# Optimization experiments

Hardware: AMD Instinct MI355X
Metric: run time of the kernel (lower is better)

Reference implementation:

```python
import jax, jax.numpy as jnp
import numpy as np

N_NODES = 40000


def gcn_conv(x, edge_index, W, b, num_nodes):
    """PyG GCNConv: add self-loops, sym-normalize, x @ W.T then scatter-add, + bias."""
    src = edge_index[0]
    dst = edge_index[1]
    loop = jnp.arange(num_nodes, dtype=src.dtype)
    src = jnp.concatenate([src, loop])
    dst = jnp.concatenate([dst, loop])
    # linear transform first (PyG applies lin before propagate)
    h = x @ W.T  # [N, out]
    # symmetric normalization: deg over destination (with self-loops)
    deg = jax.ops.segment_sum(jnp.ones_like(dst, dtype=h.dtype), dst, num_segments=num_nodes)
    dinv = jnp.where(deg > 0, jax.lax.rsqrt(deg), 0.0)
    norm = dinv[src] * dinv[dst]  # [E+N]
    msg = h[src] * norm[:, None]  # gather + scale
    out = jax.ops.segment_sum(msg, dst, num_segments=num_nodes)  # scatter-add
    return out + b


def setup_inputs() -> dict:
    key = jax.random.key(0)
    k1, k2, k3, k4, k5, k6, k7 = jax.random.split(key, 7)
    C, H, F_out = 128, 128, 1
    E = 640000
    x = jax.random.normal(k1, (N_NODES, C), dtype=jnp.float32)
    edge_index = jax.random.randint(k2, (2, E), 0, N_NODES, dtype=jnp.int64)
    # Glorot-ish init for conv weights (PyG lin.weight shape [out, in]), zero bias
    W1 = jax.random.normal(k3, (H, C), dtype=jnp.float32) / np.sqrt(C)
    b1 = jnp.zeros((H,), dtype=jnp.float32)
    W2 = jax.random.normal(k4, (F_out, H), dtype=jnp.float32) / np.sqrt(H)
    b2 = jnp.zeros((F_out,), dtype=jnp.float32)
    return {"x": x, "edge_index": edge_index, "W1": W1, "b1": b1, "W2": W2, "b2": b2}


def reference(x, edge_index, W1, b1, W2, b2):
    h = gcn_conv(x, edge_index, W1, b1, N_NODES)
    h = jax.nn.relu(h)
    out = gcn_conv(h, edge_index, W2, b2, N_NODES)
    return jax.nn.sigmoid(out)
```

## Files before the change

### kernel.cpp

```cpp
#include <hip/hip_runtime.h>
#include <math.h>
#include <stdint.h>

#define FDIM 128
#define CAP 64

typedef __bf16 bf16x8 __attribute__((ext_vector_type(8)));
typedef float f32x4 __attribute__((ext_vector_type(4)));

__device__ __forceinline__ ushort f2bf(float f) {
    uint32_t u = __float_as_uint(f);
    uint32_t r = (u >> 16) & 1;
    return (ushort)((u + 0x7fffu + r) >> 16);
}


__global__ __launch_bounds__(256) void k_zero4(int4* __restrict__ p, int n4) {
    int i = blockIdx.x * blockDim.x + threadIdx.x;
    int stride = gridDim.x * blockDim.x;
    for (; i < n4; i += stride) p[i] = make_int4(0, 0, 0, 0);
}

__global__ __launch_bounds__(256) void k_scatter_ell(const int* __restrict__ src,
                                                     const int* __restrict__ dst,
                                                     int* __restrict__ cnt,
                                                     ushort* __restrict__ ell, int E) {
    int e = blockIdx.x * blockDim.x + threadIdx.x;
    if (e < E) {
        int d = dst[e];
        int p = atomicAdd(&cnt[d], 1);
        if (p < CAP) ell[(size_t)d * CAP + p] = (ushort)src[e];
    }
}


#define XS 136

__global__ __launch_bounds__(256) void k_linear1_mfma(const float* __restrict__ x,
                                                      const float* __restrict__ W,
                                                      const int* __restrict__ cnt,
                                                      ushort* __restrict__ h, int n) {
    __shared__ __align__(16) ushort Wl[128 * XS];
    __shared__ __align__(16) ushort Xl[64 * XS];

    int tid = threadIdx.x;
    int node0 = blockIdx.x * 64;

#pragma unroll
    for (int i = 0; i < 16; ++i) {
        int q = tid + i * 256;
        int j = q >> 5;
        int c0 = (q & 31) * 4;
        float4 v = *(const float4*)(W + (size_t)q * 4);
        uint2 p;
        p.x = (uint32_t)f2bf(v.x) | ((uint32_t)f2bf(v.y) << 16);
        p.y = (uint32_t)f2bf(v.z) | ((uint32_t)f2bf(v.w) << 16);
        *(uint2*)&Wl[j * XS + c0] = p;
    }
#pragma unroll
    for (int i = 0; i < 8; ++i) {
        int q = tid + i * 256;
        int r = q >> 5;
        int c0 = (q & 31) * 4;
        int gr = node0 + r;
        float4 v = make_float4(0.f, 0.f, 0.f, 0.f);
        float s = 0.f;
        if (gr < n) {
            v = *(const float4*)(x + (size_t)gr * FDIM + c0);
            s = rsqrtf((float)cnt[gr] + 1.0f);
        }
        uint2 p;
        p.x = (uint32_t)f2bf(v.x * s) | ((uint32_t)f2bf(v.y * s) << 16);
        p.y = (uint32_t)f2bf(v.z * s) | ((uint32_t)f2bf(v.w * s) << 16);
        *(uint2*)&Xl[r * XS + c0] = p;
    }
    __syncthreads();

    int lane = tid & 63, wid = tid >> 6;
    int m0 = (wid >> 1) * 32;
    int j0 = (wid & 1) * 64;
    int lrow = lane & 15, kg = lane >> 4;

    bf16x8 af[2][4];
#pragma unroll
    for (int mt = 0; mt < 2; ++mt)
#pragma unroll
        for (int ks = 0; ks < 4; ++ks)
            af[mt][ks] = *(const bf16x8*)&Xl[(m0 + mt * 16 + lrow) * XS + ks * 32 + kg * 8];

    f32x4 acc[2][4] = {};
#pragma unroll
    for (int jt = 0; jt < 4; ++jt) {
        bf16x8 bfr[4];
#pragma unroll
        for (int ks = 0; ks < 4; ++ks)
            bfr[ks] = *(const bf16x8*)&Wl[(j0 + jt * 16 + lrow) * XS + ks * 32 + kg * 8];
#pragma unroll
        for (int mt = 0; mt < 2; ++mt)
#pragma unroll
            for (int ks = 0; ks < 4; ++ks)
                acc[mt][jt] = __builtin_amdgcn_mfma_f32_16x16x32_bf16(
                    af[mt][ks], bfr[ks], acc[mt][jt], 0, 0, 0);
    }

#pragma unroll
    for (int mt = 0; mt < 2; ++mt)
#pragma unroll
        for (int jt = 0; jt < 4; ++jt)
#pragma unroll
            for (int r = 0; r < 4; ++r) {
                int gi = node0 + m0 + mt * 16 + kg * 4 + r;
                int gj = j0 + jt * 16 + lrow;
                if (gi < n) h[(size_t)gi * FDIM + gj] = f2bf(acc[mt][jt][r]);
            }
}


__device__ __forceinline__ float bf_lo(uint32_t u) { return __uint_as_float(u << 16); }
__device__ __forceinline__ float bf_hi(uint32_t u) { return __uint_as_float(u & 0xFFFF0000u); }

__global__ __launch_bounds__(256) void k_agg1_h2(const uint32_t* __restrict__ h,
                                                 const ushort* __restrict__ ell,
                                                 const int* __restrict__ cnt,
                                                 const float* __restrict__ b1,
                                                 const float* __restrict__ W2,
                                                 float* __restrict__ h2s, int n) {
    int gtid = blockIdx.x * blockDim.x + threadIdx.x;
    int d = gtid >> 6;
    int lane = threadIdx.x & 63;
    if (d >= n) return;

    int degt = cnt[d];
    int deg = min(degt, CAP);
    int myidx = (lane < deg) ? (int)ell[(size_t)d * CAP + lane] : 0;

    uint32_t u = h[(size_t)d * 64 + lane];
    float ax[8], ay[8];
    ax[0] = bf_lo(u); ay[0] = bf_hi(u);
#pragma unroll
    for (int r = 1; r < 8; ++r) { ax[r] = 0.f; ay[r] = 0.f; }

    int k = 0;
    for (; k + 7 < deg; k += 8) {
        int s[8];
        uint32_t uu[8];
#pragma unroll
        for (int r = 0; r < 8; ++r) s[r] = __shfl(myidx, k + r);
#pragma unroll
        for (int r = 0; r < 8; ++r) uu[r] = h[(size_t)s[r] * 64 + lane];
#pragma unroll
        for (int r = 0; r < 8; ++r) { ax[r] += bf_lo(uu[r]); ay[r] += bf_hi(uu[r]); }
    }
    for (; k + 3 < deg; k += 4) {
        int s[4];
        uint32_t uu[4];
#pragma unroll
        for (int r = 0; r < 4; ++r) s[r] = __shfl(myidx, k + r);
#pragma unroll
        for (int r = 0; r < 4; ++r) uu[r] = h[(size_t)s[r] * 64 + lane];
#pragma unroll
        for (int r = 0; r < 4; ++r) { ax[r] += bf_lo(uu[r]); ay[r] += bf_hi(uu[r]); }
    }
    for (; k < deg; ++k) {
        int s0 = __shfl(myidx, k);
        uint32_t u0 = h[(size_t)s0 * 64 + lane];
        ax[0] += bf_lo(u0); ay[0] += bf_hi(u0);
    }

    float sx = ((ax[0] + ax[1]) + (ax[2] + ax[3])) + ((ax[4] + ax[5]) + (ax[6] + ax[7]));
    float sy = ((ay[0] + ay[1]) + (ay[2] + ay[3])) + ((ay[4] + ay[5]) + (ay[6] + ay[7]));

    float dd = rsqrtf((float)degt + 1.0f);
    float ox = sx * dd;
    float oy = sy * dd;

    float2 bb = *(const float2*)(b1 + lane * 2);
    float2 ww = *(const float2*)(W2 + lane * 2);
    float s = fmaxf(ox + bb.x, 0.f) * ww.x + fmaxf(oy + bb.y, 0.f) * ww.y;
#pragma unroll
    for (int o = 32; o; o >>= 1) s += __shfl_down(s, o);
    if (lane == 0) h2s[d] = s * dd;
}


__global__ __launch_bounds__(256) void k_agg2(const float* __restrict__ h2s,
                                              const ushort* __restrict__ ell,
                                              const int* __restrict__ cnt,
                                              const float* __restrict__ b2,
                                              float* __restrict__ out, int n) {
    int gtid = blockIdx.x * blockDim.x + threadIdx.x;
    int i = gtid >> 6;
    int lane = threadIdx.x & 63;
    if (i >= n) return;

    int degt = cnt[i];
    int deg = min(degt, CAP);
    float v = 0.f;
    if (lane < deg) {
        int s = ell[(size_t)i * CAP + lane];
        v = h2s[s];
    }
#pragma unroll
    for (int o = 32; o; o >>= 1) v += __shfl_down(v, o);
    if (lane == 0) {
        float dd = rsqrtf((float)degt + 1.0f);
        float r = (h2s[i] + v) * dd + b2[0];
        out[i] = 1.f / (1.f + expf(-r));
    }
}


extern "C" void kernel_launch(void* const* d_in, const int* in_sizes, int n_in,
                              void* d_out, int out_size, void* d_ws, size_t ws_size,
                              hipStream_t stream) {
    const float* x  = (const float*)d_in[0];
    const int*   ei = (const int*)d_in[1];
    const float* W1 = (const float*)d_in[2];
    const float* b1 = (const float*)d_in[3];
    const float* W2 = (const float*)d_in[4];
    const float* b2 = (const float*)d_in[5];

    int n = out_size;
    int E = in_sizes[1] / 2;
    const int* src = ei;
    const int* dst = ei + E;

    char* w = (char*)d_ws;
    int*    cnt = (int*)w;     w += (size_t)((n + 3) & ~3) * 4;
    ushort* ell = (ushort*)w;  w += (size_t)n * CAP * 2;
    ushort* h1s = (ushort*)w;  w += (size_t)n * FDIM * 2;
    float*  h2s = (float*)w;   w += (size_t)n * 4;

    int n4 = ((n + 3) & ~3) / 4;

    k_zero4<<<40, 256, 0, stream>>>((int4*)cnt, n4);
    k_scatter_ell<<<(E + 255) / 256, 256, 0, stream>>>(src, dst, cnt, ell, E);
    k_linear1_mfma<<<(n + 63) / 64, 256, 0, stream>>>(x, W1, cnt, h1s, n);
    k_agg1_h2<<<(n * 64 + 255) / 256, 256, 0, stream>>>((const uint32_t*)h1s, ell, cnt, b1, W2, h2s, n);
    k_agg2<<<(n * 64 + 255) / 256, 256, 0, stream>>>(h2s, ell, cnt, b2, (float*)d_out, n);
}
```

Measured before the change: 85.38 us.

## Fold count zeroing into linear kernel, move source normalization into aggregation

Zeroing the degree counters now happens inside the linear kernel, which also drops its dependence on counts and runs before the edge scatter. The per-source degree scaling moves from the linear stage into the first aggregation kernel, where each lane gathers its neighbour's count and shares it by shuffle. The linear kernel now handles two 64-node tiles per block so each staged W tile is reused. The scatter kernel reads four edges per thread with vector loads. The aim is to remove one launch and break the count dependency; the cost is an extra per-edge count gather and multiply in aggregation.

```diff
diff --git a/kernel.cpp b/kernel.cpp
--- a/kernel.cpp
+++ b/kernel.cpp
@@ -15,36 +15,21 @@
 }
 
 
-__global__ __launch_bounds__(256) void k_zero4(int4* __restrict__ p, int n4) {
-    int i = blockIdx.x * blockDim.x + threadIdx.x;
-    int stride = gridDim.x * blockDim.x;
-    for (; i < n4; i += stride) p[i] = make_int4(0, 0, 0, 0);
-}
-
-__global__ __launch_bounds__(256) void k_scatter_ell(const int* __restrict__ src,
-                                                     const int* __restrict__ dst,
-                                                     int* __restrict__ cnt,
-                                                     ushort* __restrict__ ell, int E) {
-    int e = blockIdx.x * blockDim.x + threadIdx.x;
-    if (e < E) {
-        int d = dst[e];
-        int p = atomicAdd(&cnt[d], 1);
-        if (p < CAP) ell[(size_t)d * CAP + p] = (ushort)src[e];
-    }
-}
-
-
 #define XS 136
 
 __global__ __launch_bounds__(256) void k_linear1_mfma(const float* __restrict__ x,
                                                       const float* __restrict__ W,
-                                                      const int* __restrict__ cnt,
+                                                      int* __restrict__ cnt,
                                                       ushort* __restrict__ h, int n) {
     __shared__ __align__(16) ushort Wl[128 * XS];
     __shared__ __align__(16) ushort Xl[64 * XS];
 
     int tid = threadIdx.x;
-    int node0 = blockIdx.x * 64;
+
+    if (tid < 128) {
+        int g = blockIdx.x * 128 + tid;
+        if (g < n) cnt[g] = 0;
+    }
 
 #pragma unroll
     for (int i = 0; i < 16; ++i) {
@@ -57,62 +42,89 @@
         p.y = (uint32_t)f2bf(v.z) | ((uint32_t)f2bf(v.w) << 16);
         *(uint2*)&Wl[j * XS + c0] = p;
     }
-#pragma unroll
-    for (int i = 0; i < 8; ++i) {
-        int q = tid + i * 256;
-        int r = q >> 5;
-        int c0 = (q & 31) * 4;
-        int gr = node0 + r;
-        float4 v = make_float4(0.f, 0.f, 0.f, 0.f);
-        float s = 0.f;
-        if (gr < n) {
-            v = *(const float4*)(x + (size_t)gr * FDIM + c0);
-            s = rsqrtf((float)cnt[gr] + 1.0f);
-        }
-        uint2 p;
-        p.x = (uint32_t)f2bf(v.x * s) | ((uint32_t)f2bf(v.y * s) << 16);
-        p.y = (uint32_t)f2bf(v.z * s) | ((uint32_t)f2bf(v.w * s) << 16);
-        *(uint2*)&Xl[r * XS + c0] = p;
-    }
-    __syncthreads();
 
     int lane = tid & 63, wid = tid >> 6;
     int m0 = (wid >> 1) * 32;
     int j0 = (wid & 1) * 64;
     int lrow = lane & 15, kg = lane >> 4;
 
-    bf16x8 af[2][4];
-#pragma unroll
-    for (int mt = 0; mt < 2; ++mt)
-#pragma unroll
-        for (int ks = 0; ks < 4; ++ks)
-            af[mt][ks] = *(const bf16x8*)&Xl[(m0 + mt * 16 + lrow) * XS + ks * 32 + kg * 8];
-
-    f32x4 acc[2][4] = {};
-#pragma unroll
-    for (int jt = 0; jt < 4; ++jt) {
-        bf16x8 bfr[4];
-#pragma unroll
-        for (int ks = 0; ks < 4; ++ks)
-            bfr[ks] = *(const bf16x8*)&Wl[(j0 + jt * 16 + lrow) * XS + ks * 32 + kg * 8];
+    for (int t = 0; t < 2; ++t) {
+        int node0 = blockIdx.x * 128 + t * 64;
+        if (node0 >= n) break;
+
+        __syncthreads();
+#pragma unroll
+        for (int i = 0; i < 8; ++i) {
+            int q = tid + i * 256;
+            int r = q >> 5;
+            int c0 = (q & 31) * 4;
+            int gr = node0 + r;
+            float4 v = make_float4(0.f, 0.f, 0.f, 0.f);
+            if (gr < n) v = *(const float4*)(x + (size_t)gr * FDIM + c0);
+            uint2 p;
+            p.x = (uint32_t)f2bf(v.x) | ((uint32_t)f2bf(v.y) << 16);
+            p.y = (uint32_t)f2bf(v.z) | ((uint32_t)f2bf(v.w) << 16);
+            *(uint2*)&Xl[r * XS + c0] = p;
+        }
+        __syncthreads();
+
+        bf16x8 af[2][4];
 #pragma unroll
         for (int mt = 0; mt < 2; ++mt)
 #pragma unroll
             for (int ks = 0; ks < 4; ++ks)
-                acc[mt][jt] = __builtin_amdgcn_mfma_f32_16x16x32_bf16(
-                    af[mt][ks], bfr[ks], acc[mt][jt], 0, 0, 0);
-    }
-
-#pragma unroll
-    for (int mt = 0; mt < 2; ++mt)
-#pragma unroll
-        for (int jt = 0; jt < 4; ++jt)
-#pragma unroll
-            for (int r = 0; r < 4; ++r) {
-                int gi = node0 + m0 + mt * 16 + kg * 4 + r;
-                int gj = j0 + jt * 16 + lrow;
-                if (gi < n) h[(size_t)gi * FDIM + gj] = f2bf(acc[mt][jt][r]);
-            }
+                af[mt][ks] = *(const bf16x8*)&Xl[(m0 + mt * 16 + lrow) * XS + ks * 32 + kg * 8];
+
+        f32x4 acc[2][4] = {};
+#pragma unroll
+        for (int jt = 0; jt < 4; ++jt) {
+            bf16x8 bfr[4];
+#pragma unroll
+            for (int ks = 0; ks < 4; ++ks)
+                bfr[ks] = *(const bf16x8*)&Wl[(j0 + jt * 16 + lrow) * XS + ks * 32 + kg * 8];
+#pragma unroll
+            for (int mt = 0; mt < 2; ++mt)
+#pragma unroll
+                for (int ks = 0; ks < 4; ++ks)
+                    acc[mt][jt] = __builtin_amdgcn_mfma_f32_16x16x32_bf16(
+                        af[mt][ks], bfr[ks], acc[mt][jt], 0, 0, 0);
+        }
+
+#pragma unroll
+        for (int mt = 0; mt < 2; ++mt)
+#pragma unroll
+            for (int jt = 0; jt < 4; ++jt)
+#pragma unroll
+                for (int r = 0; r < 4; ++r) {
+                    int gi = node0 + m0 + mt * 16 + kg * 4 + r;
+                    int gj = j0 + jt * 16 + lrow;
+                    if (gi < n) h[(size_t)gi * FDIM + gj] = f2bf(acc[mt][jt][r]);
+                }
+    }
+}
+
+
+__global__ __launch_bounds__(256) void k_scatter_ell(const int* __restrict__ src,
+                                                     const int* __restrict__ dst,
+                                                     int* __restrict__ cnt,
+                                                     ushort* __restrict__ ell, int E) {
+    int i = blockIdx.x * blockDim.x + threadIdx.x;
+    int base = i * 4;
+    if (base + 3 < E) {
+        int4 s4 = *(const int4*)(src + base);
+        int4 d4 = *(const int4*)(dst + base);
+        int p;
+        p = atomicAdd(&cnt[d4.x], 1); if (p < CAP) ell[(size_t)d4.x * CAP + p] = (ushort)s4.x;
+        p = atomicAdd(&cnt[d4.y], 1); if (p < CAP) ell[(size_t)d4.y * CAP + p] = (ushort)s4.y;
+        p = atomicAdd(&cnt[d4.z], 1); if (p < CAP) ell[(size_t)d4.z * CAP + p] = (ushort)s4.z;
+        p = atomicAdd(&cnt[d4.w], 1); if (p < CAP) ell[(size_t)d4.w * CAP + p] = (ushort)s4.w;
+    } else {
+        for (int e = base; e < E; ++e) {
+            int d = dst[e];
+            int p = atomicAdd(&cnt[d], 1);
+            if (p < CAP) ell[(size_t)d * CAP + p] = (ushort)src[e];
+        }
+    }
 }
 
 
@@ -132,45 +144,49 @@
 
     int degt = cnt[d];
     int deg = min(degt, CAP);
-    int myidx = (lane < deg) ? (int)ell[(size_t)d * CAP + lane] : 0;
-
+    int myidx = 0;
+    float mydv = 0.f;
+    if (lane < deg) {
+        myidx = (int)ell[(size_t)d * CAP + lane];
+        mydv = rsqrtf((float)cnt[myidx] + 1.0f);
+    }
+
+    float dd = rsqrtf((float)degt + 1.0f);
     uint32_t u = h[(size_t)d * 64 + lane];
     float ax[8], ay[8];
-    ax[0] = bf_lo(u); ay[0] = bf_hi(u);
+    ax[0] = bf_lo(u) * dd; ay[0] = bf_hi(u) * dd;
 #pragma unroll
     for (int r = 1; r < 8; ++r) { ax[r] = 0.f; ay[r] = 0.f; }
 
     int k = 0;
     for (; k + 7 < deg; k += 8) {
-        int s[8];
-        uint32_t uu[8];
-#pragma unroll
-        for (int r = 0; r < 8; ++r) s[r] = __shfl(myidx, k + r);
+        int s[8]; float dv[8]; uint32_t uu[8];
+#pragma unroll
+        for (int r = 0; r < 8; ++r) { s[r] = __shfl(myidx, k + r); dv[r] = __shfl(mydv, k + r); }
 #pragma unroll
         for (int r = 0; r < 8; ++r) uu[r] = h[(size_t)s[r] * 64 + lane];
 #pragma unroll
-        for (int r = 0; r < 8; ++r) { ax[r] += bf_lo(uu[r]); ay[r] += bf_hi(uu[r]); }
+        for (int r = 0; r < 8; ++r) { ax[r] += bf_lo(uu[r]) * dv[r]; ay[r] += bf_hi(uu[r]) * dv[r]; }
     }
     for (; k + 3 < deg; k += 4) {
-        int s[4];
-        uint32_t uu[4];
-#pragma unroll
-        for (int r = 0; r < 4; ++r) s[r] = __shfl(myidx, k + r);
+        int s[4]; float dv[4]; uint32_t uu[4];
+#pragma unroll
+        for (int r = 0; r < 4; ++r) { s[r] = __shfl(myidx, k + r); dv[r] = __shfl(mydv, k + r); }
 #pragma unroll
         for (int r = 0; r < 4; ++r) uu[r] = h[(size_t)s[r] * 64 + lane];
 #pragma unroll
-        for (int r = 0; r < 4; ++r) { ax[r] += bf_lo(uu[r]); ay[r] += bf_hi(uu[r]); }
+        for (int r = 0; r < 4; ++r) { ax[r] += bf_lo(uu[r]) * dv[r]; ay[r] += bf_hi(uu[r]) * dv[r]; }
     }
     for (; k < deg; ++k) {
         int s0 = __shfl(myidx, k);
+        float dv0 = __shfl(mydv, k);
         uint32_t u0 = h[(size_t)s0 * 64 + lane];
-        ax[0] += bf_lo(u0); ay[0] += bf_hi(u0);
+        ax[0] += bf_lo(u0) * dv0; ay[0] += bf_hi(u0) * dv0;
     }
 
     float sx = ((ax[0] + ax[1]) + (ax[2] + ax[3])) + ((ax[4] + ax[5]) + (ax[6] + ax[7]));
     float sy = ((ay[0] + ay[1]) + (ay[2] + ay[3])) + ((ay[4] + ay[5]) + (ay[6] + ay[7]));
 
-    float dd = rsqrtf((float)degt + 1.0f);
     float ox = sx * dd;
     float oy = sy * dd;
 
@@ -231,11 +247,11 @@
     ushort* h1s = (ushort*)w;  w += (size_t)n * FDIM * 2;
     float*  h2s = (float*)w;   w += (size_t)n * 4;
 
-    int n4 = ((n + 3) & ~3) / 4;
-
-    k_zero4<<<40, 256, 0, stream>>>((int4*)cnt, n4);
-    k_scatter_ell<<<(E + 255) / 256, 256, 0, stream>>>(src, dst, cnt, ell, E);
-    k_linear1_mfma<<<(n + 63) / 64, 256, 0, stream>>>(x, W1, cnt, h1s, n);
+    int nblk_lin = (n + 127) / 128;
+    int nblk_sc  = (E / 4 + 255) / 256;
+
+    k_linear1_mfma<<<nblk_lin, 256, 0, stream>>>(x, W1, cnt, h1s, n);
+    k_scatter_ell<<<nblk_sc, 256, 0, stream>>>(src, dst, cnt, ell, E);
     k_agg1_h2<<<(n * 64 + 255) / 256, 256, 0, stream>>>((const uint32_t*)h1s, ell, cnt, b1, W2, h2s, n);
     k_agg2<<<(n * 64 + 255) / 256, 256, 0, stream>>>(h2s, ell, cnt, b2, (float*)d_out, n);
 }
```

Measured after the change: 89.16 us. 1.04x slower.
